# Optimization experiments

Measured on AMD Instinct MI355X. Metric: run time of the kernel, lower is better.

The kernel has to match this reference:

```python
import jax, jax.numpy as jnp
import numpy as np
from math import sqrt

B, L, D_MODEL = 4, 128, 256
V, D_WORD = 50257, 768
H = 8  # n_heads; d_keys = D_MODEL // H = 32


def setup_inputs() -> dict:
    key = jax.random.key(0)
    ks = jax.random.split(key, 10)
    s = lambda k, shape, fan: jax.random.normal(k, shape, dtype=jnp.float32) / np.sqrt(fan)
    return {
        "time_series_embedding": jax.random.normal(ks[0], (B, L, D_MODEL), dtype=jnp.float32),
        "word_embedding": jax.random.normal(ks[1], (V, D_WORD), dtype=jnp.float32) * 0.02,
        "Wq": s(ks[2], (D_MODEL, D_MODEL), D_MODEL),
        "bq": jnp.zeros((D_MODEL,), jnp.float32),
        "Wk": s(ks[3], (D_WORD, D_MODEL), D_WORD),
        "bk": jnp.zeros((D_MODEL,), jnp.float32),
        "Wv": s(ks[4], (D_WORD, D_MODEL), D_WORD),
        "bv": jnp.zeros((D_MODEL,), jnp.float32),
        "Wo": s(ks[5], (D_MODEL, D_MODEL), D_MODEL),
        "bo": jnp.zeros((D_MODEL,), jnp.float32),
    }


def reference(time_series_embedding, word_embedding, Wq, bq, Wk, bk, Wv, bv, Wo, bo):
    b, l, _ = time_series_embedding.shape
    v, _ = word_embedding.shape
    h = H
    e = D_MODEL // h
    # projections
    query = (time_series_embedding @ Wq + bq).reshape(b, l, h, e)   # [B,L,H,E]
    key = (word_embedding @ Wk + bk).reshape(v, h, e)               # [V,H,E]
    value = (word_embedding @ Wv + bv).reshape(v, h, e)             # [V,H,E]
    scale = 1.0 / sqrt(e)
    # scores over full vocab: [B,H,V,L]
    scores = jnp.einsum('blhe,vhe->bhvl', query, key)
    # NOTE: faithful to source -- softmax over the LAST axis (l, the query dim)
    attn = jax.nn.softmax(scale * scores, axis=-1)
    # dropout is identity in eval mode
    reprog = jnp.einsum('bhvl,vhe->blhe', attn, value).reshape(b, l, h * e)
    return reprog @ Wo + bo  # [B,L,d_model]
```

## Files before the change

kernel.cpp:

```cpp
#include <hip/hip_runtime.h>
#include <hip/hip_bf16.h>
#include <string.h>

#define BB 4
#define LL 128
#define DM 256
#define VV 50257
#define VPAD 50304
#define DW 768
#define HH 8
#define EE 32

typedef __attribute__((ext_vector_type(8))) short sh8;
typedef __attribute__((ext_vector_type(4))) short sh4;
typedef __attribute__((ext_vector_type(4))) float f32x4;

static __device__ inline unsigned short bfbits(float x) {
  __hip_bfloat16 h = __float2bfloat16(x);
  unsigned short u;
  __builtin_memcpy(&u, &h, 2);
  return u;
}

static __device__ inline sh8 ld8_b64(const short* p) {
  sh4 lo = *(const sh4*)p;
  sh4 hi = *(const sh4*)(p + 4);
  return __builtin_shufflevector(lo, hi, 0, 1, 2, 3, 4, 5, 6, 7);
}

__global__ __launch_bounds__(256) void qproj_kernel(
    const float* __restrict__ tse, const float* __restrict__ Wq,
    const float* __restrict__ bq, unsigned short* __restrict__ Qb) {
  __shared__ float row[DM];
  int r = blockIdx.x;
  int n = threadIdx.x;
  row[n] = tse[r * DM + n];
  __syncthreads();
  float acc = bq[n];
#pragma unroll 8
  for (int k = 0; k < DM; ++k)
    acc = fmaf(row[k], Wq[k * DM + n], acc);
  const float scale = 0.17677669529663687f;
  Qb[r * DM + n] = bfbits(acc * scale);
}

__global__ __launch_bounds__(256) void wtrans_kernel(
    const float* __restrict__ Wk, const float* __restrict__ Wv,
    unsigned short* __restrict__ Wkt, unsigned short* __restrict__ Wvt) {
  __shared__ float tileS[64][65];
  const float* src = blockIdx.z ? Wv : Wk;
  unsigned short* dst = blockIdx.z ? Wvt : Wkt;
  int k0 = blockIdx.x * 64, n0 = blockIdx.y * 64;
  int t = threadIdx.x;
  int c = t & 63, rb = t >> 6;
#pragma unroll
  for (int j = 0; j < 16; ++j) {
    int r = j * 4 + rb;
    tileS[r][c] = src[(size_t)(k0 + r) * DM + n0 + c];
  }
  __syncthreads();
#pragma unroll
  for (int j = 0; j < 16; ++j) {
    int r = j * 4 + rb;
    dst[(size_t)(n0 + r) * DW + k0 + c] = bfbits(tileS[c][r]);
  }
}

#define KST2 36
__global__ __launch_bounds__(256, 2) void kvproj_kernel(
    const float* __restrict__ WE, const unsigned short* __restrict__ Wkt,
    const unsigned short* __restrict__ Wvt, const float* __restrict__ bk,
    const float* __restrict__ bv, unsigned short* __restrict__ Kb,
    unsigned short* __restrict__ Vb) {
  __shared__ short WEb[128 * KST2];
  __shared__ short Wkb[128 * KST2];
  __shared__ short Wvb[128 * KST2];

  int bx = blockIdx.x;
  int v0 = (bx >> 1) * 128;
  int colbase = (bx & 1) * 128;
  int t = threadIdx.x;
  int w = t >> 6, lane = t & 63, a = lane & 15, quad = lane >> 4;
  int wm = w >> 1, wn = w & 1;
  int sr = t >> 1;
  int skc = (t & 1) * 16;
  const bool live = (v0 + sr) < VV;

  float4 a0, a1, a2, a3;
  sh8 k0, k1, x0, x1;

  auto issue_loads = [&](int kt) {
    if (live) {
      const float* wep = WE + (size_t)(v0 + sr) * DW + kt * 32 + skc;
      a0 = *(const float4*)(wep + 0);
      a1 = *(const float4*)(wep + 4);
      a2 = *(const float4*)(wep + 8);
      a3 = *(const float4*)(wep + 12);
    } else {
      a0 = a1 = a2 = a3 = (float4){0.f, 0.f, 0.f, 0.f};
    }
    const unsigned short* kp = Wkt + (size_t)(colbase + sr) * DW + kt * 32 + skc;
    const unsigned short* vp = Wvt + (size_t)(colbase + sr) * DW + kt * 32 + skc;
    k0 = *(const sh8*)(kp + 0);
    k1 = *(const sh8*)(kp + 8);
    x0 = *(const sh8*)(vp + 0);
    x1 = *(const sh8*)(vp + 8);
  };

  f32x4 Ck[4][4], Cv[4][4];
#pragma unroll
  for (int mb = 0; mb < 4; ++mb)
#pragma unroll
    for (int nb = 0; nb < 4; ++nb) {
      Ck[mb][nb] = (f32x4){0.f, 0.f, 0.f, 0.f};
      Cv[mb][nb] = (f32x4){0.f, 0.f, 0.f, 0.f};
    }

  issue_loads(0);

  for (int kt = 0; kt < 24; ++kt) {
    __syncthreads();

    {
      sh4 w0 = {(short)bfbits(a0.x), (short)bfbits(a0.y),
                (short)bfbits(a0.z), (short)bfbits(a0.w)};
      sh4 w1 = {(short)bfbits(a1.x), (short)bfbits(a1.y),
                (short)bfbits(a1.z), (short)bfbits(a1.w)};
      sh4 w2 = {(short)bfbits(a2.x), (short)bfbits(a2.y),
                (short)bfbits(a2.z), (short)bfbits(a2.w)};
      sh4 w3 = {(short)bfbits(a3.x), (short)bfbits(a3.y),
                (short)bfbits(a3.z), (short)bfbits(a3.w)};
      short* eb = &WEb[sr * KST2 + skc];
      *(sh4*)(eb + 0) = w0;
      *(sh4*)(eb + 4) = w1;
      *(sh4*)(eb + 8) = w2;
      *(sh4*)(eb + 12) = w3;
      short* kb = &Wkb[sr * KST2 + skc];
      *(sh4*)(kb + 0) = __builtin_shufflevector(k0, k0, 0, 1, 2, 3);
      *(sh4*)(kb + 4) = __builtin_shufflevector(k0, k0, 4, 5, 6, 7);
      *(sh4*)(kb + 8) = __builtin_shufflevector(k1, k1, 0, 1, 2, 3);
      *(sh4*)(kb + 12) = __builtin_shufflevector(k1, k1, 4, 5, 6, 7);
      short* vb = &Wvb[sr * KST2 + skc];
      *(sh4*)(vb + 0) = __builtin_shufflevector(x0, x0, 0, 1, 2, 3);
      *(sh4*)(vb + 4) = __builtin_shufflevector(x0, x0, 4, 5, 6, 7);
      *(sh4*)(vb + 8) = __builtin_shufflevector(x1, x1, 0, 1, 2, 3);
      *(sh4*)(vb + 12) = __builtin_shufflevector(x1, x1, 4, 5, 6, 7);
    }
    __syncthreads();

    if (kt < 23) issue_loads(kt + 1);

    sh8 A[4], Bk[4], Bv[4];
#pragma unroll
    for (int mb = 0; mb < 4; ++mb)
      A[mb] = ld8_b64(&WEb[(wm * 64 + mb * 16 + a) * KST2 + quad * 8]);
#pragma unroll
    for (int nb = 0; nb < 4; ++nb) {
      Bk[nb] = ld8_b64(&Wkb[((wn * 4 + nb) * 16 + a) * KST2 + quad * 8]);
      Bv[nb] = ld8_b64(&Wvb[((wn * 4 + nb) * 16 + a) * KST2 + quad * 8]);
    }
#pragma unroll
    for (int mb = 0; mb < 4; ++mb)
#pragma unroll
      for (int nb = 0; nb < 4; ++nb) {
        Ck[mb][nb] = __builtin_amdgcn_mfma_f32_16x16x32_bf16(
            A[mb], Bk[nb], Ck[mb][nb], 0, 0, 0);
        Cv[mb][nb] = __builtin_amdgcn_mfma_f32_16x16x32_bf16(
            A[mb], Bv[nb], Cv[mb][nb], 0, 0, 0);
      }
  }

  float bkv[4], bvv[4];
#pragma unroll
  for (int nb = 0; nb < 4; ++nb) {
    int n = colbase + (wn * 4 + nb) * 16 + a;
    bkv[nb] = bk[n];
    bvv[nb] = bv[n];
  }
#pragma unroll
  for (int mb = 0; mb < 4; ++mb)
#pragma unroll
    for (int nb = 0; nb < 4; ++nb)
#pragma unroll
      for (int r = 0; r < 4; ++r) {
        int m = v0 + wm * 64 + mb * 16 + quad * 4 + r;
        int n = colbase + (wn * 4 + nb) * 16 + a;
        bool ok = m < VV;
        Kb[(size_t)m * DM + n] = ok ? bfbits(Ck[mb][nb][r] + bkv[nb]) : 0;
        Vb[(size_t)m * DM + n] = ok ? bfbits(Cv[mb][nb][r] + bvv[nb]) : 0;
      }
}

__global__ void zero_kernel(float* __restrict__ p, int n) {
  int i = blockIdx.x * blockDim.x + threadIdx.x;
  if (i < n) p[i] = 0.f;
}

#define PST 72
__global__ __launch_bounds__(256) void attn_kernel(
    const unsigned short* __restrict__ Qb, const unsigned short* __restrict__ Kb,
    const unsigned short* __restrict__ Vb, float* __restrict__ reprog, int bpb) {
  __shared__ short Pb[LL * PST];
  __shared__ short Vt[EE * PST];

  int bh = blockIdx.x / bpb;
  int chunk = blockIdx.x - bh * bpb;
  int b = bh >> 3, h = bh & 7;
  int t = threadIdx.x;
  int w = t >> 6;
  int lane = t & 63;
  int a = lane & 15;
  int quad = lane >> 4;
  int vr = t >> 2, e0 = (t & 3) * 8;

  sh8 qf[8];
  const unsigned short* qbase = Qb + (size_t)(b * LL) * DM + h * EE;
#pragma unroll
  for (int tau = 0; tau < 8; ++tau)
    qf[tau] = *(const sh8*)(qbase + (size_t)(tau * 16 + a) * DM + quad * 8);

  f32x4 C[2][2];
#pragma unroll
  for (int mb = 0; mb < 2; ++mb)
#pragma unroll
    for (int nb = 0; nb < 2; ++nb)
      C[mb][nb] = (f32x4){0.f, 0.f, 0.f, 0.f};

  const int ntiles = VPAD >> 6;

  sh8 af, vv;
  {
    int v0 = chunk << 6;
    af = *(const sh8*)(Kb + (size_t)(v0 + 16 * w + a) * DM + h * EE + quad * 8);
    vv = *(const sh8*)(Vb + (size_t)(v0 + vr) * DM + h * EE + e0);
  }

  for (int tile = chunk; tile < ntiles; tile += bpb) {
    f32x4 S[8];
#pragma unroll
    for (int tau = 0; tau < 8; ++tau) {
      f32x4 z = {0.f, 0.f, 0.f, 0.f};
      S[tau] = __builtin_amdgcn_mfma_f32_16x16x32_bf16(af, qf[tau], z, 0, 0, 0);
    }

    float mx[4], sm[4], inv[4];
#pragma unroll
    for (int r = 0; r < 4; ++r) {
      float m = S[0][r];
#pragma unroll
      for (int tau = 1; tau < 8; ++tau) m = fmaxf(m, S[tau][r]);
      mx[r] = m;
    }
#pragma unroll
    for (int msk = 1; msk <= 8; msk <<= 1)
#pragma unroll
      for (int r = 0; r < 4; ++r)
        mx[r] = fmaxf(mx[r], __shfl_xor(mx[r], msk));
#pragma unroll
    for (int r = 0; r < 4; ++r) sm[r] = 0.f;
#pragma unroll
    for (int tau = 0; tau < 8; ++tau)
#pragma unroll
      for (int r = 0; r < 4; ++r) {
        float ex = __expf(S[tau][r] - mx[r]);
        S[tau][r] = ex;
        sm[r] += ex;
      }
#pragma unroll
    for (int msk = 1; msk <= 8; msk <<= 1)
#pragma unroll
      for (int r = 0; r < 4; ++r)
        sm[r] += __shfl_xor(sm[r], msk);
#pragma unroll
    for (int r = 0; r < 4; ++r) inv[r] = 1.f / sm[r];

    __syncthreads();

    {
      const short* vs = (const short*)&vv;
#pragma unroll
      for (int j = 0; j < 8; ++j)
        Vt[(e0 + j) * PST + vr] = vs[j];
    }
#pragma unroll
    for (int tau = 0; tau < 8; ++tau) {
      ushort4 pk;
      pk.x = bfbits(S[tau][0] * inv[0]);
      pk.y = bfbits(S[tau][1] * inv[1]);
      pk.z = bfbits(S[tau][2] * inv[2]);
      pk.w = bfbits(S[tau][3] * inv[3]);
      *(ushort4*)&Pb[(tau * 16 + a) * PST + 16 * w + quad * 4] = pk;
    }
    __syncthreads();

    int nt = tile + bpb;
    if (nt < ntiles) {
      int v0n = nt << 6;
      af = *(const sh8*)(Kb + (size_t)(v0n + 16 * w + a) * DM + h * EE + quad * 8);
      vv = *(const sh8*)(Vb + (size_t)(v0n + vr) * DM + h * EE + e0);
    }

    sh8 Afr[2][2], Bfr[2][2];
#pragma unroll
    for (int mb = 0; mb < 2; ++mb)
#pragma unroll
      for (int kb = 0; kb < 2; ++kb)
        Afr[mb][kb] =
            *(const sh8*)&Pb[(32 * w + mb * 16 + a) * PST + kb * 32 + quad * 8];
#pragma unroll
    for (int kb = 0; kb < 2; ++kb)
#pragma unroll
      for (int nb = 0; nb < 2; ++nb)
        Bfr[kb][nb] = *(const sh8*)&Vt[(nb * 16 + a) * PST + kb * 32 + quad * 8];
#pragma unroll
    for (int kb = 0; kb < 2; ++kb)
#pragma unroll
      for (int mb = 0; mb < 2; ++mb)
#pragma unroll
        for (int nb = 0; nb < 2; ++nb)
          C[mb][nb] = __builtin_amdgcn_mfma_f32_16x16x32_bf16(
              Afr[mb][kb], Bfr[kb][nb], C[mb][nb], 0, 0, 0);
  }

#pragma unroll
  for (int mb = 0; mb < 2; ++mb)
#pragma unroll
    for (int nb = 0; nb < 2; ++nb)
#pragma unroll
      for (int r = 0; r < 4; ++r) {
        int l = 32 * w + mb * 16 + quad * 4 + r;
        int e = nb * 16 + a;
        atomicAdd(&reprog[(size_t)(b * LL + l) * DM + h * EE + e], C[mb][nb][r]);
      }
}

__global__ __launch_bounds__(256) void outproj_kernel(
    const float* __restrict__ reprog, const float* __restrict__ Wo,
    const float* __restrict__ bo, float* __restrict__ out) {
  __shared__ float row[DM];
  int r = blockIdx.x, n = threadIdx.x;
  row[n] = reprog[r * DM + n];
  __syncthreads();
  float acc = bo[n];
#pragma unroll 8
  for (int k = 0; k < DM; ++k)
    acc = fmaf(row[k], Wo[k * DM + n], acc);
  out[r * DM + n] = acc;
}

extern "C" void kernel_launch(void* const* d_in, const int* in_sizes, int n_in,
                              void* d_out, int out_size, void* d_ws, size_t ws_size,
                              hipStream_t stream) {
  const float* tse = (const float*)d_in[0];
  const float* WE  = (const float*)d_in[1];
  const float* Wq  = (const float*)d_in[2];
  const float* bq  = (const float*)d_in[3];
  const float* Wk  = (const float*)d_in[4];
  const float* bk  = (const float*)d_in[5];
  const float* Wv  = (const float*)d_in[6];
  const float* bv  = (const float*)d_in[7];
  const float* Wo  = (const float*)d_in[8];
  const float* bo  = (const float*)d_in[9];
  float* out = (float*)d_out;

  char* ws = (char*)d_ws;
  const size_t QB_BYTES = (size_t)BB * LL * DM * 2;
  const size_t KV_BYTES = (size_t)VPAD * DM * 2;
  const size_t WT_BYTES = (size_t)DM * DW * 2;
  unsigned short* Qb  = (unsigned short*)ws;
  unsigned short* Kb  = (unsigned short*)(ws + QB_BYTES);
  unsigned short* Vb  = (unsigned short*)(ws + QB_BYTES + KV_BYTES);
  char* X = ws + QB_BYTES + 2 * KV_BYTES;
  unsigned short* Wkt = (unsigned short*)X;
  unsigned short* Wvt = (unsigned short*)(X + WT_BYTES);
  float* reprog = (float*)X;

  const int BPB = 32;

  wtrans_kernel<<<dim3(DW / 64, DM / 64, 2), 256, 0, stream>>>(Wk, Wv, Wkt, Wvt);
  qproj_kernel<<<BB * LL, 256, 0, stream>>>(tse, Wq, bq, Qb);
  kvproj_kernel<<<(VPAD / 128) * 2, 256, 0, stream>>>(WE, Wkt, Wvt, bk, bv, Kb, Vb);
  zero_kernel<<<(BB * LL * DM + 255) / 256, 256, 0, stream>>>(reprog, BB * LL * DM);
  attn_kernel<<<32 * BPB, 256, 0, stream>>>(Qb, Kb, Vb, reprog, BPB);
  outproj_kernel<<<BB * LL, 256, 0, stream>>>(reprog, Wo, bo, out);
}
```

Measured before the change: 419.7 us.

## Double-buffer LDS in K/V projection and prefetch next tile earlier in attention

The K/V projection kernel moves from a single LDS buffer to two ping-pong buffers, with global loads issued two stages ahead so each k-step needs one barrier instead of two. The attention kernel issues the next tile's K and V loads right after the score MFMAs instead of after the softmax barrier, giving them more time to land. Costs are doubled LDS use (about 55 KB per block at launch bounds of 2 blocks) and more live registers for the extra load set, which may lower occupancy or cause spills.

```diff
diff --git a/kernel.cpp b/kernel.cpp
--- a/kernel.cpp
+++ b/kernel.cpp
@@ -67,14 +67,96 @@
 }
 
 #define KST2 36
+struct LoadSet {
+  float4 e0, e1, e2, e3;
+  sh8 k0, k1, v0, v1;
+};
+
+static __device__ inline LoadSet issue_loads(
+    const float* __restrict__ WE, const unsigned short* __restrict__ Wkt,
+    const unsigned short* __restrict__ Wvt, int v0, int colbase, int sr,
+    int skc, bool live, int kt) {
+  LoadSet s;
+  if (live) {
+    const float* wep = WE + (size_t)(v0 + sr) * DW + kt * 32 + skc;
+    s.e0 = *(const float4*)(wep + 0);
+    s.e1 = *(const float4*)(wep + 4);
+    s.e2 = *(const float4*)(wep + 8);
+    s.e3 = *(const float4*)(wep + 12);
+  } else {
+    s.e0 = s.e1 = s.e2 = s.e3 = (float4){0.f, 0.f, 0.f, 0.f};
+  }
+  const unsigned short* kp = Wkt + (size_t)(colbase + sr) * DW + kt * 32 + skc;
+  const unsigned short* vp = Wvt + (size_t)(colbase + sr) * DW + kt * 32 + skc;
+  s.k0 = *(const sh8*)(kp + 0);
+  s.k1 = *(const sh8*)(kp + 8);
+  s.v0 = *(const sh8*)(vp + 0);
+  s.v1 = *(const sh8*)(vp + 8);
+  return s;
+}
+
+static __device__ inline void store_tile(short* __restrict__ WEb,
+                                         short* __restrict__ Wkb,
+                                         short* __restrict__ Wvb, int sr,
+                                         int skc, const LoadSet& s) {
+  sh4 w0 = {(short)bfbits(s.e0.x), (short)bfbits(s.e0.y),
+            (short)bfbits(s.e0.z), (short)bfbits(s.e0.w)};
+  sh4 w1 = {(short)bfbits(s.e1.x), (short)bfbits(s.e1.y),
+            (short)bfbits(s.e1.z), (short)bfbits(s.e1.w)};
+  sh4 w2 = {(short)bfbits(s.e2.x), (short)bfbits(s.e2.y),
+            (short)bfbits(s.e2.z), (short)bfbits(s.e2.w)};
+  sh4 w3 = {(short)bfbits(s.e3.x), (short)bfbits(s.e3.y),
+            (short)bfbits(s.e3.z), (short)bfbits(s.e3.w)};
+  short* eb = &WEb[sr * KST2 + skc];
+  *(sh4*)(eb + 0) = w0;
+  *(sh4*)(eb + 4) = w1;
+  *(sh4*)(eb + 8) = w2;
+  *(sh4*)(eb + 12) = w3;
+  short* kb = &Wkb[sr * KST2 + skc];
+  *(sh4*)(kb + 0) = __builtin_shufflevector(s.k0, s.k0, 0, 1, 2, 3);
+  *(sh4*)(kb + 4) = __builtin_shufflevector(s.k0, s.k0, 4, 5, 6, 7);
+  *(sh4*)(kb + 8) = __builtin_shufflevector(s.k1, s.k1, 0, 1, 2, 3);
+  *(sh4*)(kb + 12) = __builtin_shufflevector(s.k1, s.k1, 4, 5, 6, 7);
+  short* vb = &Wvb[sr * KST2 + skc];
+  *(sh4*)(vb + 0) = __builtin_shufflevector(s.v0, s.v0, 0, 1, 2, 3);
+  *(sh4*)(vb + 4) = __builtin_shufflevector(s.v0, s.v0, 4, 5, 6, 7);
+  *(sh4*)(vb + 8) = __builtin_shufflevector(s.v1, s.v1, 0, 1, 2, 3);
+  *(sh4*)(vb + 12) = __builtin_shufflevector(s.v1, s.v1, 4, 5, 6, 7);
+}
+
+static __device__ inline void mfma_step(const short* __restrict__ WEb,
+                                        const short* __restrict__ Wkb,
+                                        const short* __restrict__ Wvb, int wm,
+                                        int wn, int a, int quad,
+                                        f32x4 Ck[4][4], f32x4 Cv[4][4]) {
+  sh8 A[4], Bk[4], Bv[4];
+#pragma unroll
+  for (int mb = 0; mb < 4; ++mb)
+    A[mb] = ld8_b64(&WEb[(wm * 64 + mb * 16 + a) * KST2 + quad * 8]);
+#pragma unroll
+  for (int nb = 0; nb < 4; ++nb) {
+    Bk[nb] = ld8_b64(&Wkb[((wn * 4 + nb) * 16 + a) * KST2 + quad * 8]);
+    Bv[nb] = ld8_b64(&Wvb[((wn * 4 + nb) * 16 + a) * KST2 + quad * 8]);
+  }
+#pragma unroll
+  for (int mb = 0; mb < 4; ++mb)
+#pragma unroll
+    for (int nb = 0; nb < 4; ++nb) {
+      Ck[mb][nb] = __builtin_amdgcn_mfma_f32_16x16x32_bf16(A[mb], Bk[nb],
+                                                           Ck[mb][nb], 0, 0, 0);
+      Cv[mb][nb] = __builtin_amdgcn_mfma_f32_16x16x32_bf16(A[mb], Bv[nb],
+                                                           Cv[mb][nb], 0, 0, 0);
+    }
+}
+
 __global__ __launch_bounds__(256, 2) void kvproj_kernel(
     const float* __restrict__ WE, const unsigned short* __restrict__ Wkt,
     const unsigned short* __restrict__ Wvt, const float* __restrict__ bk,
     const float* __restrict__ bv, unsigned short* __restrict__ Kb,
     unsigned short* __restrict__ Vb) {
-  __shared__ short WEb[128 * KST2];
-  __shared__ short Wkb[128 * KST2];
-  __shared__ short Wvb[128 * KST2];
+  __shared__ short WEb[2][128 * KST2];
+  __shared__ short Wkb[2][128 * KST2];
+  __shared__ short Wvb[2][128 * KST2];
 
   int bx = blockIdx.x;
   int v0 = (bx >> 1) * 128;
@@ -86,27 +168,6 @@
   int skc = (t & 1) * 16;
   const bool live = (v0 + sr) < VV;
 
-  float4 a0, a1, a2, a3;
-  sh8 k0, k1, x0, x1;
-
-  auto issue_loads = [&](int kt) {
-    if (live) {
-      const float* wep = WE + (size_t)(v0 + sr) * DW + kt * 32 + skc;
-      a0 = *(const float4*)(wep + 0);
-      a1 = *(const float4*)(wep + 4);
-      a2 = *(const float4*)(wep + 8);
-      a3 = *(const float4*)(wep + 12);
-    } else {
-      a0 = a1 = a2 = a3 = (float4){0.f, 0.f, 0.f, 0.f};
-    }
-    const unsigned short* kp = Wkt + (size_t)(colbase + sr) * DW + kt * 32 + skc;
-    const unsigned short* vp = Wvt + (size_t)(colbase + sr) * DW + kt * 32 + skc;
-    k0 = *(const sh8*)(kp + 0);
-    k1 = *(const sh8*)(kp + 8);
-    x0 = *(const sh8*)(vp + 0);
-    x1 = *(const sh8*)(vp + 8);
-  };
-
   f32x4 Ck[4][4], Cv[4][4];
 #pragma unroll
   for (int mb = 0; mb < 4; ++mb)
@@ -116,58 +177,22 @@
       Cv[mb][nb] = (f32x4){0.f, 0.f, 0.f, 0.f};
     }
 
-  issue_loads(0);
-
-  for (int kt = 0; kt < 24; ++kt) {
+  LoadSet sA = issue_loads(WE, Wkt, Wvt, v0, colbase, sr, skc, live, 0);
+  LoadSet sB = issue_loads(WE, Wkt, Wvt, v0, colbase, sr, skc, live, 1);
+  store_tile(WEb[0], Wkb[0], Wvb[0], sr, skc, sA);
+
+  for (int kt = 0; kt < 24; kt += 2) {
     __syncthreads();
-
-    {
-      sh4 w0 = {(short)bfbits(a0.x), (short)bfbits(a0.y),
-                (short)bfbits(a0.z), (short)bfbits(a0.w)};
-      sh4 w1 = {(short)bfbits(a1.x), (short)bfbits(a1.y),
-                (short)bfbits(a1.z), (short)bfbits(a1.w)};
-      sh4 w2 = {(short)bfbits(a2.x), (short)bfbits(a2.y),
-                (short)bfbits(a2.z), (short)bfbits(a2.w)};
-      sh4 w3 = {(short)bfbits(a3.x), (short)bfbits(a3.y),
-                (short)bfbits(a3.z), (short)bfbits(a3.w)};
-      short* eb = &WEb[sr * KST2 + skc];
-      *(sh4*)(eb + 0) = w0;
-      *(sh4*)(eb + 4) = w1;
-      *(sh4*)(eb + 8) = w2;
-      *(sh4*)(eb + 12) = w3;
-      short* kb = &Wkb[sr * KST2 + skc];
-      *(sh4*)(kb + 0) = __builtin_shufflevector(k0, k0, 0, 1, 2, 3);
-      *(sh4*)(kb + 4) = __builtin_shufflevector(k0, k0, 4, 5, 6, 7);
-      *(sh4*)(kb + 8) = __builtin_shufflevector(k1, k1, 0, 1, 2, 3);
-      *(sh4*)(kb + 12) = __builtin_shufflevector(k1, k1, 4, 5, 6, 7);
-      short* vb = &Wvb[sr * KST2 + skc];
-      *(sh4*)(vb + 0) = __builtin_shufflevector(x0, x0, 0, 1, 2, 3);
-      *(sh4*)(vb + 4) = __builtin_shufflevector(x0, x0, 4, 5, 6, 7);
-      *(sh4*)(vb + 8) = __builtin_shufflevector(x1, x1, 0, 1, 2, 3);
-      *(sh4*)(vb + 12) = __builtin_shufflevector(x1, x1, 4, 5, 6, 7);
-    }
+    mfma_step(WEb[0], Wkb[0], Wvb[0], wm, wn, a, quad, Ck, Cv);
+    if (kt + 2 < 24)
+      sA = issue_loads(WE, Wkt, Wvt, v0, colbase, sr, skc, live, kt + 2);
+    store_tile(WEb[1], Wkb[1], Wvb[1], sr, skc, sB);
     __syncthreads();
-
-    if (kt < 23) issue_loads(kt + 1);
-
-    sh8 A[4], Bk[4], Bv[4];
-#pragma unroll
-    for (int mb = 0; mb < 4; ++mb)
-      A[mb] = ld8_b64(&WEb[(wm * 64 + mb * 16 + a) * KST2 + quad * 8]);
-#pragma unroll
-    for (int nb = 0; nb < 4; ++nb) {
-      Bk[nb] = ld8_b64(&Wkb[((wn * 4 + nb) * 16 + a) * KST2 + quad * 8]);
-      Bv[nb] = ld8_b64(&Wvb[((wn * 4 + nb) * 16 + a) * KST2 + quad * 8]);
-    }
-#pragma unroll
-    for (int mb = 0; mb < 4; ++mb)
-#pragma unroll
-      for (int nb = 0; nb < 4; ++nb) {
-        Ck[mb][nb] = __builtin_amdgcn_mfma_f32_16x16x32_bf16(
-            A[mb], Bk[nb], Ck[mb][nb], 0, 0, 0);
-        Cv[mb][nb] = __builtin_amdgcn_mfma_f32_16x16x32_bf16(
-            A[mb], Bv[nb], Cv[mb][nb], 0, 0, 0);
-      }
+    mfma_step(WEb[1], Wkb[1], Wvb[1], wm, wn, a, quad, Ck, Cv);
+    if (kt + 3 < 24)
+      sB = issue_loads(WE, Wkt, Wvt, v0, colbase, sr, skc, live, kt + 3);
+    if (kt + 2 < 24)
+      store_tile(WEb[0], Wkb[0], Wvb[0], sr, skc, sA);
   }
 
   float bkv[4], bvv[4];
@@ -243,6 +268,17 @@
       S[tau] = __builtin_amdgcn_mfma_f32_16x16x32_bf16(af, qf[tau], z, 0, 0, 0);
     }
 
+    sh8 af_n, vv_n;
+    {
+      int nt = tile + bpb;
+      if (nt < ntiles) {
+        int v0n = nt << 6;
+        af_n = *(const sh8*)(Kb + (size_t)(v0n + 16 * w + a) * DM + h * EE +
+                             quad * 8);
+        vv_n = *(const sh8*)(Vb + (size_t)(v0n + vr) * DM + h * EE + e0);
+      }
+    }
+
     float mx[4], sm[4], inv[4];
 #pragma unroll
     for (int r = 0; r < 4; ++r) {
@@ -293,13 +329,6 @@
     }
     __syncthreads();
 
-    int nt = tile + bpb;
-    if (nt < ntiles) {
-      int v0n = nt << 6;
-      af = *(const sh8*)(Kb + (size_t)(v0n + 16 * w + a) * DM + h * EE + quad * 8);
-      vv = *(const sh8*)(Vb + (size_t)(v0n + vr) * DM + h * EE + e0);
-    }
-
     sh8 Afr[2][2], Bfr[2][2];
 #pragma unroll
     for (int mb = 0; mb < 2; ++mb)
@@ -320,6 +349,9 @@
         for (int nb = 0; nb < 2; ++nb)
           C[mb][nb] = __builtin_amdgcn_mfma_f32_16x16x32_bf16(
               Afr[mb][kb], Bfr[kb][nb], C[mb][nb], 0, 0, 0);
+
+    af = af_n;
+    vv = vv_n;
   }
 
 #pragma unroll
```

Measured after the change: 431.1 us. +2.7%, slower.
